# Performance work log

Measured on AMD Instinct MI355X. Metric: run time of the kernel, lower is better.

## Reference

```python
import jax, jax.numpy as jnp
import numpy as np

B, N, M = 16, 4096, 1024
INPUT_DIM, COND_DIM = 512, 512
HEADS, DIM_HEAD = 8, 64
HIDDEN = HEADS * DIM_HEAD


def setup_inputs() -> dict:
    key = jax.random.key(0)
    ks = jax.random.split(key, 6)
    x = jax.random.normal(ks[0], (B, INPUT_DIM, N), dtype=jnp.float32)
    c = jax.random.normal(ks[1], (B, COND_DIM, M), dtype=jnp.float32)
    # 1x1 conv weights as [out_ch, in_ch] matrices
    Wq = jax.random.normal(ks[2], (HIDDEN, INPUT_DIM), dtype=jnp.float32) * (INPUT_DIM ** -0.5)
    Wkv = jax.random.normal(ks[3], (2 * HIDDEN, COND_DIM), dtype=jnp.float32) * (COND_DIM ** -0.5)
    Wo = jax.random.normal(ks[4], (INPUT_DIM, HIDDEN), dtype=jnp.float32) * (HIDDEN ** -0.5)
    bo = jax.random.normal(ks[5], (INPUT_DIM,), dtype=jnp.float32) * 0.01
    return {"x": x, "c": c, "Wq": Wq, "Wkv": Wkv, "Wo": Wo, "bo": bo}


def reference(x, c, Wq, Wkv, Wo, bo):
    scale = DIM_HEAD ** -0.5
    # 1x1 convs == channel-mixing matmuls
    q = jnp.einsum('bcn,oc->bon', x, Wq)            # [B, HIDDEN, N]
    kv = jnp.einsum('bcm,oc->bom', c, Wkv)          # [B, 2*HIDDEN, M]
    k, v = jnp.split(kv, 2, axis=1)                 # each [B, HIDDEN, M]
    # split heads: b (h d) n -> b h d n
    q = q.reshape(B, HEADS, DIM_HEAD, N) * scale
    k = k.reshape(B, HEADS, DIM_HEAD, M)
    v = v.reshape(B, HEADS, DIM_HEAD, M)
    # softmax over conditioning sequence dim
    k = jax.nn.softmax(k, axis=-1)
    # context: [B, H, d, e] (dim_head x dim_head)
    context = jnp.einsum('bhdm,bhem->bhde', k, v)
    # out: [B, H, e, N]
    out = jnp.einsum('bhde,bhdn->bhen', context, q)
    out = out.reshape(B, HIDDEN, N)
    return jnp.einsum('bcn,oc->bon', out, Wo) + bo[None, :, None]
```

## Files before the change

kernel.cpp:

```cpp
#include <hip/hip_runtime.h>

#define KDIM 512

typedef __attribute__((ext_vector_type(8))) short bf16x8;
typedef __attribute__((ext_vector_type(4))) float f32x4;
typedef unsigned short u16;
typedef unsigned int u32;

static __device__ __forceinline__ u16 f2bf(float f) {
  u32 u = __builtin_bit_cast(u32, f);
  u32 r = u + 0x7fffu + ((u >> 16) & 1u);
  return (u16)(r >> 16);
}
static __device__ __forceinline__ bf16x8 ld_frag(const u16* p) {
  uint2 lo = *(const uint2*)p;
  uint2 hi = *(const uint2*)(p + 4);
  uint4 u = make_uint4(lo.x, lo.y, hi.x, hi.y);
  return __builtin_bit_cast(bf16x8, u);
}

__global__ __launch_bounds__(256) void cvt_f32_bf16(
    const float* __restrict__ src, u16* __restrict__ dst, int n8)
{
  int i = blockIdx.x * 256 + threadIdx.x;
  if (i >= n8) return;
  float4 a = *(const float4*)(src + (long)i * 8);
  float4 b = *(const float4*)(src + (long)i * 8 + 4);
  u32 w0 = (u32)f2bf(a.x) | ((u32)f2bf(a.y) << 16);
  u32 w1 = (u32)f2bf(a.z) | ((u32)f2bf(a.w) << 16);
  u32 w2 = (u32)f2bf(b.x) | ((u32)f2bf(b.y) << 16);
  u32 w3 = (u32)f2bf(b.z) | ((u32)f2bf(b.w) << 16);
  *(uint4*)(dst + (long)i * 8) = make_uint4(w0, w1, w2, w3);
}

template<bool OUT_BF16, bool BIAS, int MT, int NT>
__global__ __launch_bounds__(512, 4) void gemm_v3(
    const u16* __restrict__ Ap, long a_bstride,
    const float* __restrict__ Bp, long b_bstride,
    void* __restrict__ Op, long o_bstride,
    const float* __restrict__ bias, int ldn)
{
  constexpr int LDT = 68;
  __shared__ u16 Ash[256 * LDT];
  __shared__ u16 Bsh[128 * LDT];

  const int d = blockIdx.x;
  const int mt = d % MT;
  const int nt = (d / MT) % NT;
  const int b  = d / (MT * NT);
  const long mtile = (long)mt * 256;
  const long ntile = (long)nt * 128;
  const u16* Ab = Ap + (long)b * a_bstride + mtile * KDIM;
  const float* Bb = Bp + (long)b * b_bstride + ntile;

  const int t = threadIdx.x;
  const int lane = t & 63, wv = t >> 6;
  const int wm = wv >> 1, wn = wv & 1;
  const int lrow = lane & 15, lkh = lane >> 4;

  const int ar = t >> 3, ac8 = t & 7;
  const int nq = t & 31;
  const int kq = t >> 5;

  f32x4 acc[4][4] = {};
  uint4 pa[4];
  float4 pb[4];

  #define LOADA_V3(kt) { _Pragma("unroll") \
    for (int i_ = 0; i_ < 4; ++i_) \
      pa[i_] = *(const uint4*)(Ab + (long)(ar + i_ * 64) * KDIM + (kt) + ac8 * 8); }

  #define LOADB_V3(kt) { _Pragma("unroll") \
    for (int k_ = 0; k_ < 4; ++k_) \
      pb[k_] = *(const float4*)(Bb + (long)((kt) + kq * 4 + k_) * ldn + nq * 4); }

  #define STAGE_V3() { \
    _Pragma("unroll") for (int i_ = 0; i_ < 4; ++i_) { \
      u16* dst_ = &Ash[(ar + i_ * 64) * LDT + ac8 * 8]; \
      *(uint2*)dst_       = make_uint2(pa[i_].x, pa[i_].y); \
      *(uint2*)(dst_ + 4) = make_uint2(pa[i_].z, pa[i_].w); } \
    float q0_[4] = {pb[0].x, pb[0].y, pb[0].z, pb[0].w}; \
    float q1_[4] = {pb[1].x, pb[1].y, pb[1].z, pb[1].w}; \
    float q2_[4] = {pb[2].x, pb[2].y, pb[2].z, pb[2].w}; \
    float q3_[4] = {pb[3].x, pb[3].y, pb[3].z, pb[3].w}; \
    _Pragma("unroll") for (int j_ = 0; j_ < 4; ++j_) { \
      u32 w0_ = (u32)f2bf(q0_[j_]) | ((u32)f2bf(q1_[j_]) << 16); \
      u32 w1_ = (u32)f2bf(q2_[j_]) | ((u32)f2bf(q3_[j_]) << 16); \
      *(uint2*)&Bsh[(nq * 4 + j_) * LDT + kq * 4] = make_uint2(w0_, w1_); } }

  LOADA_V3(0) LOADB_V3(0)
  STAGE_V3()
  __syncthreads();

  for (int s = 0; s < 8; ++s) {
    if (s < 7) { LOADA_V3((s + 1) * 64) LOADB_V3((s + 1) * 64) }
    #pragma unroll
    for (int kk = 0; kk < 2; ++kk) {
      bf16x8 bfr[4];
      #pragma unroll
      for (int ni = 0; ni < 4; ++ni)
        bfr[ni] = ld_frag(&Bsh[(wn * 64 + ni * 16 + lrow) * LDT + kk * 32 + lkh * 8]);
      #pragma unroll
      for (int mi = 0; mi < 4; ++mi) {
        bf16x8 af = ld_frag(&Ash[(wm * 64 + mi * 16 + lrow) * LDT + kk * 32 + lkh * 8]);
        #pragma unroll
        for (int ni = 0; ni < 4; ++ni)
          acc[mi][ni] = __builtin_amdgcn_mfma_f32_16x16x32_bf16(af, bfr[ni], acc[mi][ni], 0, 0, 0);
      }
    }
    __syncthreads();
    if (s < 7) {
      STAGE_V3()
      __syncthreads();
    }
  }

  #pragma unroll
  for (int mi = 0; mi < 4; ++mi) {
    #pragma unroll
    for (int r = 0; r < 4; ++r) {
      long gr = mtile + wm * 64 + mi * 16 + lkh * 4 + r;
      float bv = 0.0f;
      if constexpr (BIAS) bv = bias[gr];
      #pragma unroll
      for (int ni = 0; ni < 4; ++ni) {
        long gc = ntile + wn * 64 + ni * 16 + lrow;
        float v = acc[mi][ni][r] + bv;
        if constexpr (OUT_BF16)
          ((u16*)Op)[(long)b * o_bstride + gr * ldn + gc] = f2bf(v);
        else
          ((float*)Op)[(long)b * o_bstride + gr * ldn + gc] = v;
      }
    }
  }
  #undef LOADA_V3
  #undef LOADB_V3
  #undef STAGE_V3
}

__global__ __launch_bounds__(256, 2) void softmax_context(
    const u16* __restrict__ kv, float* __restrict__ ctx)
{
  constexpr int LDE = 132;
  __shared__ float rowmax[64], rowinv[64];
  __shared__ u16 Ke[64 * LDE];
  __shared__ u16 Vs[64 * LDE];
  __shared__ float pr[64 * 68];

  const int bh = blockIdx.x;
  const u16* Kr = kv + (long)(bh >> 3) * (1024 * 1024) + (long)(bh & 7) * (64 * 1024);
  const u16* Vr = Kr + 512 * 1024;

  const int t = threadIdx.x;
  const int lane = t & 63, wv = t >> 6;
  const int lrow = lane & 15, lkh = lane >> 4;
  const int d4 = t >> 2, q4 = t & 3;

  {
    const u16* row = Kr + d4 * 1024 + q4 * 256;
    float mx = -3e38f;
    for (int i = 0; i < 256; i += 8) {
      uint4 v = *(const uint4*)(row + i);
      u32 ws[4] = {v.x, v.y, v.z, v.w};
      #pragma unroll
      for (int j = 0; j < 4; ++j) {
        mx = fmaxf(mx, __builtin_bit_cast(float, ws[j] << 16));
        mx = fmaxf(mx, __builtin_bit_cast(float, ws[j] & 0xffff0000u));
      }
    }
    mx = fmaxf(mx, __shfl_xor(mx, 1));
    mx = fmaxf(mx, __shfl_xor(mx, 2));
    float s = 0.f;
    for (int i = 0; i < 256; i += 8) {
      uint4 v = *(const uint4*)(row + i);
      u32 ws[4] = {v.x, v.y, v.z, v.w};
      #pragma unroll
      for (int j = 0; j < 4; ++j) {
        s += __expf(__builtin_bit_cast(float, ws[j] << 16) - mx);
        s += __expf(__builtin_bit_cast(float, ws[j] & 0xffff0000u) - mx);
      }
    }
    s += __shfl_xor(s, 1);
    s += __shfl_xor(s, 2);
    if (q4 == 0) { rowmax[d4] = mx; rowinv[d4] = 1.f / s; }
  }
  __syncthreads();

  f32x4 cacc[4][4] = {};

  for (int mc = 0; mc < 8; ++mc) {
    {
      int dd = t >> 2, j = t & 3;
      int m0 = mc * 128 + j * 32;
      float mx = rowmax[dd], inv = rowinv[dd];
      const u16* src = Kr + dd * 1024 + m0;
      u16* dst = &Ke[dd * LDE + j * 32];
      #pragma unroll
      for (int cq = 0; cq < 4; ++cq) {
        uint4 v = *(const uint4*)(src + cq * 8);
        u32 in[4] = {v.x, v.y, v.z, v.w};
        u32 out[4];
        #pragma unroll
        for (int j2 = 0; j2 < 4; ++j2) {
          float lo = __builtin_bit_cast(float, in[j2] << 16);
          float hi = __builtin_bit_cast(float, in[j2] & 0xffff0000u);
          out[j2] = (u32)f2bf(__expf(lo - mx) * inv) |
                    ((u32)f2bf(__expf(hi - mx) * inv) << 16);
        }
        *(uint2*)(dst + cq * 8)     = make_uint2(out[0], out[1]);
        *(uint2*)(dst + cq * 8 + 4) = make_uint2(out[2], out[3]);
      }
      const u16* vsrc = Vr + dd * 1024 + m0;
      u16* vdst = &Vs[dd * LDE + j * 32];
      #pragma unroll
      for (int cq = 0; cq < 4; ++cq) {
        uint4 v = *(const uint4*)(vsrc + cq * 8);
        *(uint2*)(vdst + cq * 8)     = make_uint2(v.x, v.y);
        *(uint2*)(vdst + cq * 8 + 4) = make_uint2(v.z, v.w);
      }
    }
    __syncthreads();
    bf16x8 ka[4], vb[4];
    #pragma unroll
    for (int mi = 0; mi < 4; ++mi)
      ka[mi] = ld_frag(&Ke[(mi * 16 + lrow) * LDE + wv * 32 + lkh * 8]);
    #pragma unroll
    for (int ni = 0; ni < 4; ++ni)
      vb[ni] = ld_frag(&Vs[(ni * 16 + lrow) * LDE + wv * 32 + lkh * 8]);
    #pragma unroll
    for (int mi = 0; mi < 4; ++mi)
      #pragma unroll
      for (int ni = 0; ni < 4; ++ni)
        cacc[mi][ni] = __builtin_amdgcn_mfma_f32_16x16x32_bf16(ka[mi], vb[ni], cacc[mi][ni], 0, 0, 0);
    __syncthreads();
  }

  for (int w = 0; w < 4; ++w) {
    if (wv == w) {
      #pragma unroll
      for (int mi = 0; mi < 4; ++mi)
        #pragma unroll
        for (int ni = 0; ni < 4; ++ni)
          #pragma unroll
          for (int r = 0; r < 4; ++r) {
            float* p = &pr[(mi * 16 + lkh * 4 + r) * 68 + (ni * 16 + lrow)];
            float v = cacc[mi][ni][r];
            if (w == 0) *p = v; else *p += v;
          }
    }
    __syncthreads();
  }
  float* cg = ctx + (long)bh * 4096;
  for (int i = 0; i < 16; ++i) {
    int o = t + i * 256;
    cg[o] = 0.125f * pr[(o >> 6) * 68 + (o & 63)];
  }
}

__global__ __launch_bounds__(256) void compose_u(
    const float* __restrict__ ctx, const float* __restrict__ Wo, u16* __restrict__ U)
{
  __shared__ float cs[16 * 64];
  const int bh = blockIdx.x, dq = blockIdx.y;
  const int b = bh >> 3, h = bh & 7;
  const int t = threadIdx.x;
  const float* cgrp = ctx + (long)bh * 4096 + dq * 16 * 64;
  for (int i = t; i < 1024; i += 256) cs[i] = cgrp[i];
  __syncthreads();
  #pragma unroll
  for (int rep = 0; rep < 2; ++rep) {
    int o = rep * 256 + t;
    const float* wrow = Wo + (long)o * 512 + h * 64;
    float acc[16] = {};
    for (int e = 0; e < 64; ++e) {
      float w = wrow[e];
      #pragma unroll
      for (int dd = 0; dd < 16; ++dd) acc[dd] += w * cs[dd * 64 + e];
    }
    u16* urow = U + (long)b * (512 * 512) + (long)o * 512 + h * 64 + dq * 16;
    #pragma unroll
    for (int dd = 0; dd < 16; ++dd) urow[dd] = f2bf(acc[dd]);
  }
}

extern "C" void kernel_launch(void* const* d_in, const int* in_sizes, int n_in,
                              void* d_out, int out_size, void* d_ws, size_t ws_size,
                              hipStream_t stream)
{
  const float* x   = (const float*)d_in[0];
  const float* c   = (const float*)d_in[1];
  const float* Wq  = (const float*)d_in[2];
  const float* Wkv = (const float*)d_in[3];
  const float* Wo  = (const float*)d_in[4];
  const float* bo  = (const float*)d_in[5];

  char* ws = (char*)d_ws;
  u16*   kv   = (u16*)ws;
  float* ctx  = (float*)(ws + 33554432);
  u16*   U    = (u16*)(ws + 35651584);
  u16*   Weff = (u16*)(ws + 44040192);
  u16*   Wkvb = (u16*)(ws + 44040192);

  cvt_f32_bf16<<<dim3(256), 256, 0, stream>>>(Wkv, Wkvb, 65536);
  gemm_v3<true, false, 4, 8><<<dim3(4 * 8 * 16), 512, 0, stream>>>(
      Wkvb, 0, c, 512L * 1024, kv, 1024L * 1024, nullptr, 1024);
  softmax_context<<<dim3(128), 256, 0, stream>>>(kv, ctx);
  compose_u<<<dim3(128, 4), 256, 0, stream>>>(ctx, Wo, U);
  gemm_v3<true, false, 2, 4><<<dim3(2 * 4 * 16), 512, 0, stream>>>(
      U, 512L * 512, Wq, 0, Weff, 512L * 512, nullptr, 512);
  gemm_v3<false, true, 2, 32><<<dim3(2 * 32 * 16), 512, 0, stream>>>(
      Weff, 512L * 512, x, 512L * 4096, d_out, 512L * 4096, bo, 4096);
}
```

Before: 195.4 us.

## Replace LDS-staged GEMM with direct-from-global register-fragment GEMM

Replaces the shared-memory tiled GEMM with a kernel where each wave loads its A and B MFMA fragments straight from global memory, converting B from fp32 to bf16 in registers, with no LDS and no barriers. Tile shapes change to 64-column N tiles and 4 waves per block, with per-wave M strips of 64 or 128 rows, and setprio is raised around the MFMA burst. This removes LDS staging and sync overhead. The cost is uncoalesced strided scalar B loads (8 rows per fragment, 16 floats per row segment), less data reuse within a block, and more redundant global and L2 traffic.

```diff
diff --git a/kernel.cpp b/kernel.cpp
--- a/kernel.cpp
+++ b/kernel.cpp
@@ -33,98 +33,68 @@
   *(uint4*)(dst + (long)i * 8) = make_uint4(w0, w1, w2, w3);
 }
 
-template<bool OUT_BF16, bool BIAS, int MT, int NT>
-__global__ __launch_bounds__(512, 4) void gemm_v3(
+template<bool OUT_BF16, bool BIAS, int MIT, int MT, int NT>
+__global__ __launch_bounds__(256, (MIT == 4 ? 4 : 2)) void gemm_direct(
     const u16* __restrict__ Ap, long a_bstride,
     const float* __restrict__ Bp, long b_bstride,
     void* __restrict__ Op, long o_bstride,
     const float* __restrict__ bias, int ldn)
 {
-  constexpr int LDT = 68;
-  __shared__ u16 Ash[256 * LDT];
-  __shared__ u16 Bsh[128 * LDT];
-
   const int d = blockIdx.x;
   const int mt = d % MT;
   const int nt = (d / MT) % NT;
   const int b  = d / (MT * NT);
-  const long mtile = (long)mt * 256;
-  const long ntile = (long)nt * 128;
-  const u16* Ab = Ap + (long)b * a_bstride + mtile * KDIM;
-  const float* Bb = Bp + (long)b * b_bstride + ntile;
+  const long mtile = (long)mt * (4 * MIT * 16);
+  const long ntile = (long)nt * 64;
 
   const int t = threadIdx.x;
   const int lane = t & 63, wv = t >> 6;
-  const int wm = wv >> 1, wn = wv & 1;
   const int lrow = lane & 15, lkh = lane >> 4;
 
-  const int ar = t >> 3, ac8 = t & 7;
-  const int nq = t & 31;
-  const int kq = t >> 5;
-
-  f32x4 acc[4][4] = {};
-  uint4 pa[4];
-  float4 pb[4];
-
-  #define LOADA_V3(kt) { _Pragma("unroll") \
-    for (int i_ = 0; i_ < 4; ++i_) \
-      pa[i_] = *(const uint4*)(Ab + (long)(ar + i_ * 64) * KDIM + (kt) + ac8 * 8); }
-
-  #define LOADB_V3(kt) { _Pragma("unroll") \
-    for (int k_ = 0; k_ < 4; ++k_) \
-      pb[k_] = *(const float4*)(Bb + (long)((kt) + kq * 4 + k_) * ldn + nq * 4); }
-
-  #define STAGE_V3() { \
-    _Pragma("unroll") for (int i_ = 0; i_ < 4; ++i_) { \
-      u16* dst_ = &Ash[(ar + i_ * 64) * LDT + ac8 * 8]; \
-      *(uint2*)dst_       = make_uint2(pa[i_].x, pa[i_].y); \
-      *(uint2*)(dst_ + 4) = make_uint2(pa[i_].z, pa[i_].w); } \
-    float q0_[4] = {pb[0].x, pb[0].y, pb[0].z, pb[0].w}; \
-    float q1_[4] = {pb[1].x, pb[1].y, pb[1].z, pb[1].w}; \
-    float q2_[4] = {pb[2].x, pb[2].y, pb[2].z, pb[2].w}; \
-    float q3_[4] = {pb[3].x, pb[3].y, pb[3].z, pb[3].w}; \
-    _Pragma("unroll") for (int j_ = 0; j_ < 4; ++j_) { \
-      u32 w0_ = (u32)f2bf(q0_[j_]) | ((u32)f2bf(q1_[j_]) << 16); \
-      u32 w1_ = (u32)f2bf(q2_[j_]) | ((u32)f2bf(q3_[j_]) << 16); \
-      *(uint2*)&Bsh[(nq * 4 + j_) * LDT + kq * 4] = make_uint2(w0_, w1_); } }
-
-  LOADA_V3(0) LOADB_V3(0)
-  STAGE_V3()
-  __syncthreads();
-
-  for (int s = 0; s < 8; ++s) {
-    if (s < 7) { LOADA_V3((s + 1) * 64) LOADB_V3((s + 1) * 64) }
-    #pragma unroll
-    for (int kk = 0; kk < 2; ++kk) {
-      bf16x8 bfr[4];
+  const u16* Aw = Ap + (long)b * a_bstride
+                + (mtile + (long)wv * (MIT * 16) + lrow) * KDIM + lkh * 8;
+  const float* Bw = Bp + (long)b * b_bstride
+                  + (long)(lkh * 8) * ldn + ntile + lrow;
+
+  f32x4 acc[MIT][4] = {};
+
+  for (int kt = 0; kt < KDIM; kt += 32) {
+    bf16x8 af[MIT];
+    #pragma unroll
+    for (int mi = 0; mi < MIT; ++mi)
+      af[mi] = *(const bf16x8*)(Aw + (long)mi * 16 * KDIM + kt);
+    bf16x8 bfr[4];
+    #pragma unroll
+    for (int ni = 0; ni < 4; ++ni) {
+      float v[8];
+      #pragma unroll
+      for (int j = 0; j < 8; ++j)
+        v[j] = Bw[(long)(kt + j) * ldn + ni * 16];
+      u32 p0 = (u32)f2bf(v[0]) | ((u32)f2bf(v[1]) << 16);
+      u32 p1 = (u32)f2bf(v[2]) | ((u32)f2bf(v[3]) << 16);
+      u32 p2 = (u32)f2bf(v[4]) | ((u32)f2bf(v[5]) << 16);
+      u32 p3 = (u32)f2bf(v[6]) | ((u32)f2bf(v[7]) << 16);
+      bfr[ni] = __builtin_bit_cast(bf16x8, make_uint4(p0, p1, p2, p3));
+    }
+    __builtin_amdgcn_s_setprio(1);
+    #pragma unroll
+    for (int mi = 0; mi < MIT; ++mi)
       #pragma unroll
       for (int ni = 0; ni < 4; ++ni)
-        bfr[ni] = ld_frag(&Bsh[(wn * 64 + ni * 16 + lrow) * LDT + kk * 32 + lkh * 8]);
-      #pragma unroll
-      for (int mi = 0; mi < 4; ++mi) {
-        bf16x8 af = ld_frag(&Ash[(wm * 64 + mi * 16 + lrow) * LDT + kk * 32 + lkh * 8]);
-        #pragma unroll
-        for (int ni = 0; ni < 4; ++ni)
-          acc[mi][ni] = __builtin_amdgcn_mfma_f32_16x16x32_bf16(af, bfr[ni], acc[mi][ni], 0, 0, 0);
-      }
-    }
-    __syncthreads();
-    if (s < 7) {
-      STAGE_V3()
-      __syncthreads();
-    }
+        acc[mi][ni] = __builtin_amdgcn_mfma_f32_16x16x32_bf16(af[mi], bfr[ni], acc[mi][ni], 0, 0, 0);
+    __builtin_amdgcn_s_setprio(0);
   }
 
   #pragma unroll
-  for (int mi = 0; mi < 4; ++mi) {
+  for (int mi = 0; mi < MIT; ++mi) {
     #pragma unroll
     for (int r = 0; r < 4; ++r) {
-      long gr = mtile + wm * 64 + mi * 16 + lkh * 4 + r;
+      long gr = mtile + wv * (MIT * 16) + mi * 16 + lkh * 4 + r;
       float bv = 0.0f;
       if constexpr (BIAS) bv = bias[gr];
       #pragma unroll
       for (int ni = 0; ni < 4; ++ni) {
-        long gc = ntile + wn * 64 + ni * 16 + lrow;
+        long gc = ntile + ni * 16 + lrow;
         float v = acc[mi][ni][r] + bv;
         if constexpr (OUT_BF16)
           ((u16*)Op)[(long)b * o_bstride + gr * ldn + gc] = f2bf(v);
@@ -133,9 +103,6 @@
       }
     }
   }
-  #undef LOADA_V3
-  #undef LOADB_V3
-  #undef STAGE_V3
 }
 
 __global__ __launch_bounds__(256, 2) void softmax_context(
@@ -302,12 +269,12 @@
   u16*   Wkvb = (u16*)(ws + 44040192);
 
   cvt_f32_bf16<<<dim3(256), 256, 0, stream>>>(Wkv, Wkvb, 65536);
-  gemm_v3<true, false, 4, 8><<<dim3(4 * 8 * 16), 512, 0, stream>>>(
+  gemm_direct<true, false, 8, 2, 16><<<dim3(2 * 16 * 16), 256, 0, stream>>>(
       Wkvb, 0, c, 512L * 1024, kv, 1024L * 1024, nullptr, 1024);
   softmax_context<<<dim3(128), 256, 0, stream>>>(kv, ctx);
   compose_u<<<dim3(128, 4), 256, 0, stream>>>(ctx, Wo, U);
-  gemm_v3<true, false, 2, 4><<<dim3(2 * 4 * 16), 512, 0, stream>>>(
+  gemm_direct<true, false, 4, 2, 8><<<dim3(2 * 8 * 16), 256, 0, stream>>>(
       U, 512L * 512, Wq, 0, Weff, 512L * 512, nullptr, 512);
-  gemm_v3<false, true, 2, 32><<<dim3(2 * 32 * 16), 512, 0, stream>>>(
+  gemm_direct<false, true, 4, 2, 64><<<dim3(2 * 64 * 16), 256, 0, stream>>>(
       Weff, 512L * 512, x, 512L * 4096, d_out, 512L * 4096, bo, 4096);
 }
```

After: 310.6 us (median of 2 runs). +58.9%, slower.
